# Performance work log

Measured on AMD Instinct MI355X. Metric: run time of the kernel, lower is better.

Reference implementation:

```python
import jax, jax.numpy as jnp
import numpy as np

B, T, C, H, E, TOPK, DR = 2, 2048, 768, 3072, 8, 2, 24


def setup_inputs() -> dict:
    key = jax.random.key(0)
    ks = jax.random.split(key, 16)
    std = 0.02
    n = lambda k, shape, s=std: (s * jax.random.normal(k, shape)).astype(jnp.float32)
    emb = jax.random.normal(ks[3], (E, DR), dtype=jnp.float32)
    emb = emb / (jnp.linalg.norm(emb, axis=-1, keepdims=True) + 1e-8)
    return {
        "x": jax.random.normal(ks[0], (B, T, C), dtype=jnp.float32),
        "router_w": n(ks[1], (E, C)),
        "probe_w": n(ks[2], (DR, C)),
        "router_emb": emb,
        "fatigue": jnp.zeros((E,), jnp.float32),
        "energy": jnp.ones((E,), jnp.float32),
        "w_fast1": n(ks[4], (E, C, H)),
        "w_slow1": n(ks[5], (E, C, H)),
        "h_fast1": n(ks[6], (E, C, H), 0.005),
        "m_gate1": jax.random.uniform(ks[7], (E,), dtype=jnp.float32),
        "b1": jnp.zeros((E, H), jnp.float32),
        "w_fast2": n(ks[8], (E, H, C)),
        "w_slow2": n(ks[9], (E, H, C)),
        "h_fast2": n(ks[10], (E, H, C), 0.005),
        "m_gate2": jax.random.uniform(ks[11], (E,), dtype=jnp.float32),
        "b2": jnp.zeros((E, C), jnp.float32),
    }


def _normalize(v, axis=-1, eps=1e-12):
    # matches F.normalize: v / max(||v||, eps)
    return v / jnp.maximum(jnp.linalg.norm(v, axis=axis, keepdims=True), eps)


def reference(x, router_w, probe_w, router_emb, fatigue, energy,
              w_fast1, w_slow1, h_fast1, m_gate1, b1,
              w_fast2, w_slow2, h_fast2, m_gate2, b2):
    Bd, Td, Cd = x.shape
    # --- router logits with biology-inspired biases ---
    logits = jnp.einsum('btc,ec->bte', x, router_w)            # nn.Linear, no bias
    tok_proxy = x.mean(axis=-1, keepdims=True)                  # [B,T,1]
    router_gain = jnp.linalg.norm(router_emb, axis=-1)          # [E]
    base_bias = 0.02 * tok_proxy                                # broadcasts over E
    gain_bias = 0.02 * tok_proxy * router_gain                  # [B,T,E]
    tok_unit = _normalize(jnp.einsum('btc,dc->btd', x, probe_w))
    align_bias = 0.02 * jnp.einsum('btd,ed->bte', tok_unit, _normalize(router_emb))
    logits = logits + base_bias + gain_bias + align_bias + 0.1 * energy - 0.1 * fatigue
    # --- top-k gating ---
    g, idx = jax.lax.top_k(logits, TOPK)                        # [B,T,K]
    gates = jax.nn.softmax(g, axis=-1)
    N = Bd * Td
    gates_full = jnp.zeros((N, E), x.dtype).at[
        jnp.arange(N)[:, None], idx.reshape(N, TOPK)].set(gates.reshape(N, TOPK))
    flat_x = x.reshape(N, Cd)
    # --- expert dispatch: dynamic W = w_fast + m_gate*w_slow + H_fast ---
    def body(acc, p):
        wf1, ws1, hf1, mg1, bb1, wf2, ws2, hf2, mg2, bb2, ge = p
        W1 = wf1 + mg1 * ws1 + hf1                              # [C,H]
        h = jnp.square(jnp.maximum(flat_x @ W1 + bb1, 0.0))     # relu(y)^2
        W2 = wf2 + mg2 * ws2 + hf2                              # [H,C]
        y = h @ W2 + bb2
        return acc + ge[:, None] * y, None
    out, _ = jax.lax.scan(
        body, jnp.zeros((N, Cd), x.dtype),
        (w_fast1, w_slow1, h_fast1, m_gate1, b1,
         w_fast2, w_slow2, h_fast2, m_gate2, b2, gates_full.T))
    return out.reshape(Bd, Td, Cd)
```

## Files before the change

### kernel.cpp

```cpp
#include <hip/hip_runtime.h>

typedef unsigned short u16;
typedef __attribute__((ext_vector_type(8))) short short8;
typedef __attribute__((ext_vector_type(8))) unsigned short ushort8;
typedef __attribute__((ext_vector_type(4))) unsigned short ushort4v;
typedef __attribute__((ext_vector_type(4))) float f32x4;

static constexpr int Cdim = 768;
static constexpr int Hdim = 3072;
static constexpr int Edim = 8;
static constexpr int Ntok = 4096;
static constexpr int DRc  = 24;
static constexpr int NSLOT = Ntok * 2;
static constexpr int NCHUNK = 8;
static constexpr int CCH = Cdim / NCHUNK;
static constexpr int KS2 = 3;
static constexpr int KC2 = Hdim / KS2;
static constexpr int MAXROWS = 71;
static constexpr int NFC1 = MAXROWS * 24;
static constexpr int FCX = NFC1 / 8;
static constexpr int PRX = 2304 / 8;
static constexpr int SLX = FCX + PRX;
static constexpr int PXX = 768 / 8;
static constexpr int SLA = PXX + PRX;

static constexpr size_t OFF_XB   = 0;
static constexpr size_t OFF_W1T  = 6291456;
static constexpr size_t OFF_W2T  = 44040192;
static constexpr size_t OFF_HBUF = 81788928;
static constexpr size_t OFF_XT   = OFF_HBUF;
static constexpr size_t OFF_PART = OFF_HBUF + 12582912;
static constexpr size_t OFF_YB   = OFF_W1T;
static constexpr size_t OFF_TOK  = 132120576;
static constexpr size_t OFF_CNT  = 132382720;
static constexpr size_t OFF_TSLOT= 132382784;
static constexpr size_t OFF_TG   = 132448320;

__device__ __forceinline__ u16 f2bf(float f) {
  unsigned u = __builtin_bit_cast(unsigned, f);
  u += 0x7fffu + ((u >> 16) & 1u);
  return (u16)(u >> 16);
}

__device__ __forceinline__ float bf2f(u16 v) {
  unsigned u = ((unsigned)v) << 16;
  return __builtin_bit_cast(float, u);
}

__device__ __forceinline__ void gld16(const u16* g, u16* l) {
  __builtin_amdgcn_global_load_lds((const __attribute__((address_space(1))) unsigned int*)g,
                                   (__attribute__((address_space(3))) unsigned int*)l,
                                   16, 0, 0);
}

__device__ __forceinline__ int xcd_remap(int p, int nwg) {
  int q = nwg >> 3, rem = nwg & 7;
  int x = p & 7, i = p >> 3;
  return (x < rem ? x * (q + 1) : rem * (q + 1) + (x - rem) * q) + i;
}

__device__ __forceinline__ bool decode_row(const int* __restrict__ counts, int r,
                                           int& e_out, int& tokBase, int& slotOff) {
  int run = 0;
  #pragma unroll
  for (int e = 0; e < Edim; e++) {
    int ne = counts[e];
    int nb = (ne + 127) >> 7;
    if (r < nb) { e_out = e; tokBase = r << 7; slotOff = run; return true; }
    r -= nb;
    run += ne;
  }
  return false;
}

template<int R, int CCOL>
__device__ __forceinline__ void prep_wt_body(const float* __restrict__ wf,
                                             const float* __restrict__ wsl,
                                             const float* __restrict__ hf, float m,
                                             u16* __restrict__ outw, int e, int r0, int c0,
                                             unsigned* lds) {
  const size_t base = (size_t)e * R * CCOL;
  const int t = threadIdx.x;
  {
    const int rp = t >> 5;
    const int col4 = (t & 31) * 4;
    const int c2w = (t & 31) * 2;
    #pragma unroll
    for (int i = 0; i < 8; i++) {
      int r = i * 8 + rp;
      size_t idx = base + (size_t)(r0 + r) * CCOL + c0 + col4;
      float4 a = *(const float4*)(wf + idx);
      float4 b = *(const float4*)(wsl + idx);
      float4 h = *(const float4*)(hf + idx);
      unsigned u0 = (unsigned)f2bf(fmaf(m, b.x, a.x) + h.x)
                  | ((unsigned)f2bf(fmaf(m, b.y, a.y) + h.y) << 16);
      unsigned u1 = (unsigned)f2bf(fmaf(m, b.z, a.z) + h.z)
                  | ((unsigned)f2bf(fmaf(m, b.w, a.w) + h.w) << 16);
      lds[c2w * 65 + r] = u0;
      lds[(c2w + 1) * 65 + r] = u1;
    }
  }
  __syncthreads();
  {
    const int c2 = t >> 2;
    const int rseg = (t & 3) * 16;
    const unsigned* cp = lds + c2 * 65 + rseg;
    unsigned in4[16];
    #pragma unroll
    for (int j = 0; j < 4; j++)
      *reinterpret_cast<uint4*>(&in4[j * 4]) = *reinterpret_cast<const uint4*>(cp + j * 4);
    unsigned lo[8], hi[8];
    #pragma unroll
    for (int j = 0; j < 8; j++) {
      unsigned a = in4[2 * j], b = in4[2 * j + 1];
      lo[j] = (a & 0xffffu) | (b << 16);
      hi[j] = (a >> 16) | (b & 0xffff0000u);
    }
    size_t ob = ((size_t)e * CCOL + c0 + 2 * c2) * R + r0 + rseg;
    *reinterpret_cast<uint4*>(outw + ob)          = *reinterpret_cast<const uint4*>(&lo[0]);
    *reinterpret_cast<uint4*>(outw + ob + 8)      = *reinterpret_cast<const uint4*>(&lo[4]);
    *reinterpret_cast<uint4*>(outw + ob + R)      = *reinterpret_cast<const uint4*>(&hi[0]);
    *reinterpret_cast<uint4*>(outw + ob + R + 8)  = *reinterpret_cast<const uint4*>(&hi[4]);
  }
}

__global__ __launch_bounds__(256)
void fused_pre1_kernel(const float* __restrict__ x, u16* __restrict__ x16,
                       float* __restrict__ xT,
                       const float* __restrict__ wf1, const float* __restrict__ ws1,
                       const float* __restrict__ hf1, const float* __restrict__ mg1,
                       u16* __restrict__ W1T) {
  __shared__ unsigned lsbuf[64 * 65];
  const int p = blockIdx.x;
  const int xcd = p & 7, q = p >> 3;
  const int jx = (q * PXX) / SLA;
  const bool isPx = ((q + 1) * PXX) / SLA > jx;
  if (isPx) {
    int bid = xcd * PXX + jx;
    float* tile = reinterpret_cast<float*>(lsbuf);
    const int c0 = (bid % 12) * 64;
    const int t0 = (bid / 12) * 64;
    const int tid = threadIdx.x;
    const int row = tid >> 4, col = (tid & 15) * 4;
    #pragma unroll
    for (int i = 0; i < 4; i++) {
      int r = row + i * 16;
      size_t idx = (size_t)(t0 + r) * Cdim + c0 + col;
      float4 v = *(const float4*)(x + idx);
      tile[r * 65 + col + 0] = v.x; tile[r * 65 + col + 1] = v.y;
      tile[r * 65 + col + 2] = v.z; tile[r * 65 + col + 3] = v.w;
      ushort4v o = { f2bf(v.x), f2bf(v.y), f2bf(v.z), f2bf(v.w) };
      *reinterpret_cast<ushort4v*>(x16 + idx) = o;
    }
    __syncthreads();
    const int c = tid >> 2, tg = (tid & 3) * 16;
    #pragma unroll
    for (int qq = 0; qq < 4; qq++) {
      float4 w;
      w.x = tile[(tg + qq * 4 + 0) * 65 + c];
      w.y = tile[(tg + qq * 4 + 1) * 65 + c];
      w.z = tile[(tg + qq * 4 + 2) * 65 + c];
      w.w = tile[(tg + qq * 4 + 3) * 65 + c];
      *reinterpret_cast<float4*>(xT + (size_t)(c0 + c) * Ntok + t0 + tg + qq * 4) = w;
    }
  } else {
    int bid = xcd * PRX + (q - jx);
    int e = bid / 288, rem = bid % 288;
    int xx = rem % 12, yy = rem / 12;
    prep_wt_body<768, 3072>(wf1, ws1, hf1, mg1[e], W1T, e, xx * 64, yy * 128, lsbuf);
  }
}

__global__ __launch_bounds__(256)
void logits_part_kernel(const float* __restrict__ xT, const float* __restrict__ router_w,
                        const float* __restrict__ probe_w, float* __restrict__ part,
                        int* __restrict__ counts) {
  if (blockIdx.x == 0 && blockIdx.y == 0 && threadIdx.x < Edim)
    counts[threadIdx.x] = 0;
  const int t = blockIdx.x * 256 + threadIdx.x;
  const int cB = blockIdx.y * CCH;
  float racc[Edim] = {};
  float pacc[DRc] = {};
  float sacc = 0.f;
  for (int ci = 0; ci < CCH; ci++) {
    int c = cB + ci;
    float xv = xT[(size_t)c * Ntok + t];
    sacc += xv;
    #pragma unroll
    for (int ee = 0; ee < Edim; ee++) racc[ee] = fmaf(xv, router_w[ee * Cdim + c], racc[ee]);
    #pragma unroll
    for (int d = 0; d < DRc; d++) pacc[d] = fmaf(xv, probe_w[d * Cdim + c], pacc[d]);
  }
  float* pb = part + (size_t)blockIdx.y * 33 * Ntok + t;
  #pragma unroll
  for (int ee = 0; ee < Edim; ee++) pb[(size_t)ee * Ntok] = racc[ee];
  #pragma unroll
  for (int d = 0; d < DRc; d++) pb[(size_t)(8 + d) * Ntok] = pacc[d];
  pb[(size_t)32 * Ntok] = sacc;
}

__global__ __launch_bounds__(256)
void router_fin_kernel(const float* __restrict__ part, const float* __restrict__ emb,
                       const float* __restrict__ fatigue, const float* __restrict__ energy,
                       int* __restrict__ counts, int* __restrict__ tok_list,
                       int4* __restrict__ tokslot, float2* __restrict__ tokgate) {
  const int t = blockIdx.x * 256 + threadIdx.x;
  float v[33];
  #pragma unroll
  for (int o = 0; o < 33; o++) {
    float s = 0.f;
    #pragma unroll
    for (int ch = 0; ch < NCHUNK; ch++)
      s += part[((size_t)ch * 33 + o) * Ntok + t];
    v[o] = s;
  }
  const float* racc = v;
  const float* pacc = v + 8;
  float proxy = v[32] / 768.f;
  float pn2 = 0.f;
  #pragma unroll
  for (int d = 0; d < DRc; d++) pn2 += pacc[d] * pacc[d];
  float pnorm = sqrtf(pn2);
  float logitv[Edim];
  #pragma unroll
  for (int ee = 0; ee < Edim; ee++) {
    float g2 = 0.f, dote = 0.f;
    #pragma unroll
    for (int d = 0; d < DRc; d++) {
      float ev = emb[ee * DRc + d];
      g2 += ev * ev;
      dote += pacc[d] * ev;
    }
    float gain = sqrtf(g2);
    float align = dote / (fmaxf(pnorm, 1e-12f) * fmaxf(gain, 1e-12f));
    logitv[ee] = racc[ee] + 0.02f * proxy * (1.f + gain) + 0.02f * align
               + 0.1f * energy[ee] - 0.1f * fatigue[ee];
  }
  int e0 = 0; float b0v = logitv[0];
  #pragma unroll
  for (int ee = 1; ee < Edim; ee++) if (logitv[ee] > b0v) { b0v = logitv[ee]; e0 = ee; }
  int e1 = -1; float b1v = -3.4e38f;
  #pragma unroll
  for (int ee = 0; ee < Edim; ee++) if (ee != e0 && logitv[ee] > b1v) { b1v = logitv[ee]; e1 = ee; }
  float texp = expf(b1v - b0v);
  float g0 = 1.f / (1.f + texp);
  float g1 = texp / (1.f + texp);
  int p0 = atomicAdd(&counts[e0], 1);
  tok_list[e0 * Ntok + p0] = t;
  int p1 = atomicAdd(&counts[e1], 1);
  tok_list[e1 * Ntok + p1] = t;
  tokslot[t] = make_int4(e0, p0, e1, p1);
  tokgate[t] = make_float2(g0, g1);
}

__global__ __launch_bounds__(256)
void fused_fc1p2_kernel(const u16* __restrict__ x16, const u16* __restrict__ W1T,
                        const float* __restrict__ b1, const int* __restrict__ counts,
                        const int* __restrict__ tok_list, u16* __restrict__ h_buf,
                        const float* __restrict__ wf2, const float* __restrict__ ws2,
                        const float* __restrict__ hf2, const float* __restrict__ mg2,
                        u16* __restrict__ W2T) {
  __shared__ unsigned smem4[4224];
  const int p = blockIdx.x;
  const int xcd = p & 7, q = p >> 3;
  const int j = (q * FCX) / SLX;
  const bool isFc1 = ((q + 1) * FCX) / SLX > j;
  if (!isFc1) {
    int bid = xcd * PRX + (q - j);
    int e = bid / 288, rem = bid % 288;
    int xx = rem % 48, yy = rem / 48;
    prep_wt_body<3072, 768>(wf2, ws2, hf2, mg2[e], W2T, e, xx * 64, yy * 128, smem4);
    return;
  }
  u16* As = reinterpret_cast<u16*>(smem4);
  u16* Bs = As + 4096;
  int* toks = reinterpret_cast<int*>(As + 8192);
  const int l = xcd * FCX + j;
  const int r = l / 24;
  int e, tokBase, slotOff;
  if (!decode_row(counts, r, e, tokBase, slotOff)) return;
  const int hB = l % 24;
  const int n_e = counts[e];
  const int hBase = hB * 128;
  const int tid = threadIdx.x;
  if (tid < 128) {
    int s = tokBase + tid;
    toks[tid] = (s < n_e) ? tok_list[e * Ntok + s] : 0;
  }
  __syncthreads();
  const int lane = tid & 63, wv = tid >> 6;
  const int wr = wv >> 1, wc = wv & 1;
  const int sRow = lane >> 2, sSlot = lane & 3;
  const int kbOff = (sSlot ^ ((sRow >> 1) & 3)) * 8;
  const int rA0 = wv * 16 + sRow, rA1 = 64 + rA0;
  const u16* pA0 = x16 + (size_t)toks[rA0] * Cdim + kbOff;
  const u16* pA1 = x16 + (size_t)toks[rA1] * Cdim + kbOff;
  const u16* pB0 = W1T + ((size_t)e * Hdim + hBase + rA0) * Cdim + kbOff;
  const u16* pB1 = W1T + ((size_t)e * Hdim + hBase + rA1) * Cdim + kbOff;
  const int stOff = wv * 512 + lane * 8;
  const int fr = lane & 15;
  const int qsw = (((lane >> 4) ^ ((fr >> 1) & 3))) * 8;
  f32x4 acc[4][4] = {};
  for (int it = 0; it < 24; it++) {
    int k0 = it * 32;
    gld16(pA0 + k0, As + stOff);
    gld16(pA1 + k0, As + 2048 + stOff);
    gld16(pB0 + k0, Bs + stOff);
    gld16(pB1 + k0, Bs + 2048 + stOff);
    __syncthreads();
    short8 aF[4], bF[4];
    #pragma unroll
    for (int m = 0; m < 4; m++)
      aF[m] = *reinterpret_cast<const short8*>(As + (wr * 64 + m * 16 + fr) * 32 + qsw);
    #pragma unroll
    for (int n = 0; n < 4; n++)
      bF[n] = *reinterpret_cast<const short8*>(Bs + (wc * 64 + n * 16 + fr) * 32 + qsw);
    #pragma unroll
    for (int m = 0; m < 4; m++)
      #pragma unroll
      for (int n = 0; n < 4; n++)
        acc[m][n] = __builtin_amdgcn_mfma_f32_16x16x32_bf16(aF[m], bF[n], acc[m][n], 0, 0, 0);
    __syncthreads();
  }
  const int rq = (lane >> 4) * 4;
  float bias[4];
  #pragma unroll
  for (int n = 0; n < 4; n++) bias[n] = b1[(size_t)e * Hdim + hBase + wc * 64 + n * 16 + fr];
  const int rowB = slotOff + tokBase;
  #pragma unroll
  for (int m = 0; m < 4; m++) {
    #pragma unroll
    for (int j2 = 0; j2 < 4; j2++) {
      int rl = wr * 64 + m * 16 + rq + j2;
      if (tokBase + rl < n_e) {
        size_t rb = (size_t)(rowB + rl) * Hdim + hBase + wc * 64 + fr;
        #pragma unroll
        for (int n = 0; n < 4; n++) {
          float v = fmaxf(acc[m][n][j2] + bias[n], 0.f);
          h_buf[rb + n * 16] = f2bf(v * v);
        }
      }
    }
  }
}

__global__ __launch_bounds__(256)
void fc2_kernel(const u16* __restrict__ h_buf, const u16* __restrict__ W2T,
                const float* __restrict__ b2, const int* __restrict__ counts,
                u16* __restrict__ ybuf) {
  const int l = xcd_remap(blockIdx.x, MAXROWS * 18);
  const int r = l / 18;
  int e, tokBase, slotOff;
  if (!decode_row(counts, r, e, tokBase, slotOff)) return;
  const int xb = l % 18;
  const int n_e = counts[e];
  const int kch = xb / 6;
  const int cBase = (xb % 6) * 128;
  const size_t kOff = (size_t)kch * KC2;
  __shared__ u16 As[4096];
  __shared__ u16 Bs[4096];
  const int tid = threadIdx.x;
  const int lane = tid & 63, wv = tid >> 6;
  const int wr = wv >> 1, wc = wv & 1;
  const int sRow = lane >> 2, sSlot = lane & 3;
  const int kbOff = (sSlot ^ ((sRow >> 1) & 3)) * 8;
  const int rA0 = wv * 16 + sRow, rA1 = 64 + rA0;
  const int slotB = slotOff + tokBase;
  const int s0 = min(slotB + rA0, NSLOT - 1);
  const int s1 = min(slotB + rA1, NSLOT - 1);
  const u16* pA0 = h_buf + (size_t)s0 * Hdim + kOff + kbOff;
  const u16* pA1 = h_buf + (size_t)s1 * Hdim + kOff + kbOff;
  const u16* pB0 = W2T + ((size_t)e * Cdim + cBase + rA0) * Hdim + kOff + kbOff;
  const u16* pB1 = W2T + ((size_t)e * Cdim + cBase + rA1) * Hdim + kOff + kbOff;
  const int stOff = wv * 512 + lane * 8;
  const int fr = lane & 15;
  const int qsw = (((lane >> 4) ^ ((fr >> 1) & 3))) * 8;
  f32x4 acc[4][4] = {};
  for (int it = 0; it < KC2 / 32; it++) {
    int k0 = it * 32;
    gld16(pA0 + k0, &As[stOff]);
    gld16(pA1 + k0, &As[2048 + stOff]);
    gld16(pB0 + k0, &Bs[stOff]);
    gld16(pB1 + k0, &Bs[2048 + stOff]);
    __syncthreads();
    short8 aF[4], bF[4];
    #pragma unroll
    for (int m = 0; m < 4; m++)
      aF[m] = *reinterpret_cast<const short8*>(&As[(wr * 64 + m * 16 + fr) * 32 + qsw]);
    #pragma unroll
    for (int n = 0; n < 4; n++)
      bF[n] = *reinterpret_cast<const short8*>(&Bs[(wc * 64 + n * 16 + fr) * 32 + qsw]);
    #pragma unroll
    for (int m = 0; m < 4; m++)
      #pragma unroll
      for (int n = 0; n < 4; n++)
        acc[m][n] = __builtin_amdgcn_mfma_f32_16x16x32_bf16(aF[m], bF[n], acc[m][n], 0, 0, 0);
    __syncthreads();
  }
  const int rq = (lane >> 4) * 4;
  float bias[4];
  #pragma unroll
  for (int n = 0; n < 4; n++)
    bias[n] = (kch == 0) ? b2[(size_t)e * Cdim + cBase + wc * 64 + n * 16 + fr] : 0.f;
  u16* yb = ybuf + (size_t)kch * NSLOT * Cdim;
  #pragma unroll
  for (int m = 0; m < 4; m++) {
    #pragma unroll
    for (int j = 0; j < 4; j++) {
      int rl = wr * 64 + m * 16 + rq + j;
      if (tokBase + rl < n_e) {
        u16* ob = yb + (size_t)(slotB + rl) * Cdim + cBase + wc * 64 + fr;
        #pragma unroll
        for (int n = 0; n < 4; n++)
          ob[n * 16] = f2bf(acc[m][n][j] + bias[n]);
      }
    }
  }
}

__global__ __launch_bounds__(256)
void gather_kernel(const u16* __restrict__ ybuf, const int4* __restrict__ tokslot,
                   const float2* __restrict__ tokgate, const int* __restrict__ counts,
                   float* __restrict__ out) {
  const int gid = blockIdx.x * 256 + threadIdx.x;
  const int t = gid / 192;
  const int c4 = (gid - t * 192) * 4;
  int4 ts = tokslot[t];
  float2 g = tokgate[t];
  int o0 = 0, o1 = 0, run = 0;
  #pragma unroll
  for (int e = 0; e < Edim; e++) {
    if (e == ts.x) o0 = run;
    if (e == ts.z) o1 = run;
    run += counts[e];
  }
  size_t s0 = (size_t)(o0 + ts.y) * Cdim + c4;
  size_t s1 = (size_t)(o1 + ts.w) * Cdim + c4;
  const size_t K1 = (size_t)NSLOT * Cdim;
  float acc0[4] = {}, acc1[4] = {};
  #pragma unroll
  for (int k = 0; k < KS2; k++) {
    ushort4v a = *reinterpret_cast<const ushort4v*>(ybuf + k * K1 + s0);
    ushort4v b = *reinterpret_cast<const ushort4v*>(ybuf + k * K1 + s1);
    #pragma unroll
    for (int j = 0; j < 4; j++) { acc0[j] += bf2f(a[j]); acc1[j] += bf2f(b[j]); }
  }
  float4 o;
  o.x = g.x * acc0[0] + g.y * acc1[0];
  o.y = g.x * acc0[1] + g.y * acc1[1];
  o.z = g.x * acc0[2] + g.y * acc1[2];
  o.w = g.x * acc0[3] + g.y * acc1[3];
  *reinterpret_cast<float4*>(out + (size_t)t * Cdim + c4) = o;
}

extern "C" void kernel_launch(void* const* d_in, const int* in_sizes, int n_in,
                              void* d_out, int out_size, void* d_ws, size_t ws_size,
                              hipStream_t stream) {
  const float* x        = (const float*)d_in[0];
  const float* router_w = (const float*)d_in[1];
  const float* probe_w  = (const float*)d_in[2];
  const float* emb      = (const float*)d_in[3];
  const float* fatigue  = (const float*)d_in[4];
  const float* energy   = (const float*)d_in[5];
  const float* wf1      = (const float*)d_in[6];
  const float* ws1      = (const float*)d_in[7];
  const float* hf1      = (const float*)d_in[8];
  const float* mg1      = (const float*)d_in[9];
  const float* b1       = (const float*)d_in[10];
  const float* wf2      = (const float*)d_in[11];
  const float* ws2      = (const float*)d_in[12];
  const float* hf2      = (const float*)d_in[13];
  const float* mg2      = (const float*)d_in[14];
  const float* b2       = (const float*)d_in[15];
  float* out = (float*)d_out;
  char* ws = (char*)d_ws;

  u16*    x16       = (u16*)(ws + OFF_XB);
  u16*    W1T       = (u16*)(ws + OFF_W1T);
  u16*    W2T       = (u16*)(ws + OFF_W2T);
  u16*    hbuf      = (u16*)(ws + OFF_HBUF);
  float*  xT        = (float*)(ws + OFF_XT);
  float*  part      = (float*)(ws + OFF_PART);
  u16*    ybuf      = (u16*)(ws + OFF_YB);
  int*    tok_list  = (int*)(ws + OFF_TOK);
  int*    counts    = (int*)(ws + OFF_CNT);
  int4*   tokslot   = (int4*)(ws + OFF_TSLOT);
  float2* tokgate   = (float2*)(ws + OFF_TG);

  fused_pre1_kernel<<<8 * SLA, 256, 0, stream>>>(x, x16, xT,
                                                 wf1, ws1, hf1, mg1, W1T);
  logits_part_kernel<<<dim3(Ntok / 256, NCHUNK), 256, 0, stream>>>(xT, router_w, probe_w,
                                                                   part, counts);
  router_fin_kernel<<<Ntok / 256, 256, 0, stream>>>(part, emb, fatigue, energy,
                                                    counts, tok_list, tokslot, tokgate);
  fused_fc1p2_kernel<<<8 * SLX, 256, 0, stream>>>(x16, W1T, b1, counts, tok_list, hbuf,
                                                  wf2, ws2, hf2, mg2, W2T);
  fc2_kernel<<<MAXROWS * 18, 256, 0, stream>>>(hbuf, W2T, b2, counts, ybuf);
  gather_kernel<<<Ntok * 192 / 256, 256, 0, stream>>>(ybuf, tokslot, tokgate, counts, out);
  (void)in_sizes; (void)n_in; (void)out_size; (void)ws_size;
}
```

Baseline: 324.9 us.

## Fuse router logit partials into x-conversion tiles, drop transpose and logits kernel

```diff
diff --git a/kernel.cpp b/kernel.cpp
--- a/kernel.cpp
+++ b/kernel.cpp
@@ -12,8 +12,7 @@
 static constexpr int Ntok = 4096;
 static constexpr int DRc  = 24;
 static constexpr int NSLOT = Ntok * 2;
-static constexpr int NCHUNK = 8;
-static constexpr int CCH = Cdim / NCHUNK;
+static constexpr int NCH2 = 12;
 static constexpr int KS2 = 3;
 static constexpr int KC2 = Hdim / KS2;
 static constexpr int MAXROWS = 71;
@@ -28,8 +27,7 @@
 static constexpr size_t OFF_W1T  = 6291456;
 static constexpr size_t OFF_W2T  = 44040192;
 static constexpr size_t OFF_HBUF = 81788928;
-static constexpr size_t OFF_XT   = OFF_HBUF;
-static constexpr size_t OFF_PART = OFF_HBUF + 12582912;
+static constexpr size_t OFF_PART = OFF_HBUF;
 static constexpr size_t OFF_YB   = OFF_W1T;
 static constexpr size_t OFF_TOK  = 132120576;
 static constexpr size_t OFF_CNT  = 132382720;
@@ -126,11 +124,14 @@
 
 __global__ __launch_bounds__(256)
 void fused_pre1_kernel(const float* __restrict__ x, u16* __restrict__ x16,
-                       float* __restrict__ xT,
+                       const float* __restrict__ router_w, const float* __restrict__ probe_w,
+                       float* __restrict__ part, int* __restrict__ counts,
                        const float* __restrict__ wf1, const float* __restrict__ ws1,
                        const float* __restrict__ hf1, const float* __restrict__ mg1,
                        u16* __restrict__ W1T) {
   __shared__ unsigned lsbuf[64 * 65];
+  if (blockIdx.x == 0 && threadIdx.x < Edim)
+    counts[threadIdx.x] = 0;
   const int p = blockIdx.x;
   const int xcd = p & 7, q = p >> 3;
   const int jx = (q * PXX) / SLA;
@@ -138,8 +139,8 @@
   if (isPx) {
     int bid = xcd * PXX + jx;
     float* tile = reinterpret_cast<float*>(lsbuf);
-    const int c0 = (bid % 12) * 64;
-    const int t0 = (bid / 12) * 64;
+    const int c0 = (bid % NCH2) * 64;
+    const int t0 = (bid / NCH2) * 64;
     const int tid = threadIdx.x;
     const int row = tid >> 4, col = (tid & 15) * 4;
     #pragma unroll
@@ -153,50 +154,34 @@
       *reinterpret_cast<ushort4v*>(x16 + idx) = o;
     }
     __syncthreads();
-    const int c = tid >> 2, tg = (tid & 3) * 16;
-    #pragma unroll
-    for (int qq = 0; qq < 4; qq++) {
-      float4 w;
-      w.x = tile[(tg + qq * 4 + 0) * 65 + c];
-      w.y = tile[(tg + qq * 4 + 1) * 65 + c];
-      w.z = tile[(tg + qq * 4 + 2) * 65 + c];
-      w.w = tile[(tg + qq * 4 + 3) * 65 + c];
-      *reinterpret_cast<float4*>(xT + (size_t)(c0 + c) * Ntok + t0 + tg + qq * 4) = w;
-    }
+    const int tt = tid >> 2;
+    const int oq = tid & 3;
+    const float* wrow[8];
+    #pragma unroll
+    for (int k = 0; k < 8; k++) {
+      int o = oq + 4 * k;
+      wrow[k] = (o < 8) ? (router_w + (size_t)o * Cdim + c0)
+                        : (probe_w + (size_t)(o - 8) * Cdim + c0);
+    }
+    float accv[8] = {};
+    float sacc = 0.f;
+    #pragma unroll 8
+    for (int c = 0; c < 64; c++) {
+      float xv = tile[tt * 65 + c];
+      #pragma unroll
+      for (int k = 0; k < 8; k++) accv[k] = fmaf(xv, wrow[k][c], accv[k]);
+      sacc += xv;
+    }
+    float* pb = part + (size_t)(bid % NCH2) * 33 * Ntok + t0 + tt;
+    #pragma unroll
+    for (int k = 0; k < 8; k++) pb[(size_t)(oq + 4 * k) * Ntok] = accv[k];
+    if (oq == 0) pb[(size_t)32 * Ntok] = sacc;
   } else {
     int bid = xcd * PRX + (q - jx);
     int e = bid / 288, rem = bid % 288;
     int xx = rem % 12, yy = rem / 12;
     prep_wt_body<768, 3072>(wf1, ws1, hf1, mg1[e], W1T, e, xx * 64, yy * 128, lsbuf);
   }
-}
-
-__global__ __launch_bounds__(256)
-void logits_part_kernel(const float* __restrict__ xT, const float* __restrict__ router_w,
-                        const float* __restrict__ probe_w, float* __restrict__ part,
-                        int* __restrict__ counts) {
-  if (blockIdx.x == 0 && blockIdx.y == 0 && threadIdx.x < Edim)
-    counts[threadIdx.x] = 0;
-  const int t = blockIdx.x * 256 + threadIdx.x;
-  const int cB = blockIdx.y * CCH;
-  float racc[Edim] = {};
-  float pacc[DRc] = {};
-  float sacc = 0.f;
-  for (int ci = 0; ci < CCH; ci++) {
-    int c = cB + ci;
-    float xv = xT[(size_t)c * Ntok + t];
-    sacc += xv;
-    #pragma unroll
-    for (int ee = 0; ee < Edim; ee++) racc[ee] = fmaf(xv, router_w[ee * Cdim + c], racc[ee]);
-    #pragma unroll
-    for (int d = 0; d < DRc; d++) pacc[d] = fmaf(xv, probe_w[d * Cdim + c], pacc[d]);
-  }
-  float* pb = part + (size_t)blockIdx.y * 33 * Ntok + t;
-  #pragma unroll
-  for (int ee = 0; ee < Edim; ee++) pb[(size_t)ee * Ntok] = racc[ee];
-  #pragma unroll
-  for (int d = 0; d < DRc; d++) pb[(size_t)(8 + d) * Ntok] = pacc[d];
-  pb[(size_t)32 * Ntok] = sacc;
 }
 
 __global__ __launch_bounds__(256)
@@ -210,7 +195,7 @@
   for (int o = 0; o < 33; o++) {
     float s = 0.f;
     #pragma unroll
-    for (int ch = 0; ch < NCHUNK; ch++)
+    for (int ch = 0; ch < NCH2; ch++)
       s += part[((size_t)ch * 33 + o) * Ntok + t];
     v[o] = s;
   }
@@ -479,7 +464,6 @@
   u16*    W1T       = (u16*)(ws + OFF_W1T);
   u16*    W2T       = (u16*)(ws + OFF_W2T);
   u16*    hbuf      = (u16*)(ws + OFF_HBUF);
-  float*  xT        = (float*)(ws + OFF_XT);
   float*  part      = (float*)(ws + OFF_PART);
   u16*    ybuf      = (u16*)(ws + OFF_YB);
   int*    tok_list  = (int*)(ws + OFF_TOK);
@@ -487,10 +471,8 @@
   int4*   tokslot   = (int4*)(ws + OFF_TSLOT);
   float2* tokgate   = (float2*)(ws + OFF_TG);
 
-  fused_pre1_kernel<<<8 * SLA, 256, 0, stream>>>(x, x16, xT,
+  fused_pre1_kernel<<<8 * SLA, 256, 0, stream>>>(x, x16, router_w, probe_w, part, counts,
                                                  wf1, ws1, hf1, mg1, W1T);
-  logits_part_kernel<<<dim3(Ntok / 256, NCHUNK), 256, 0, stream>>>(xT, router_w, probe_w,
-                                                                   part, counts);
   router_fin_kernel<<<Ntok / 256, 256, 0, stream>>>(part, emb, fatigue, energy,
                                                     counts, tok_list, tokslot, tokgate);
   fused_fc1p2_kernel<<<8 * SLX, 256, 0, stream>>>(x16, W1T, b1, counts, tok_list, hbuf,
```

After: 432.2 us. 1.33x slower.
